# Optimization experiments

Measured on AMD Instinct MI355X. Metric: run time of the kernel, lower is better.

## Reference

```python
import jax, jax.numpy as jnp
import numpy as np
from jax import lax

NALGOS = 64
NTASKS = 1024
LX_LEN = 512
TASK_DIFFICULTY_SCALE = 1.0


def setup_inputs() -> dict:
    key = jax.random.key(0)
    k1, k2, k3, k4, k5, k6 = jax.random.split(key, 6)
    lx = jax.random.randint(k1, (LX_LEN,), 0, NTASKS)
    # task similarity in [-1, 1] as in the original (np.random.random * 2 - 1)
    task_matrix = jax.random.uniform(k2, (NTASKS, NTASKS), dtype=jnp.float32) * 2.0 - 1.0
    # difficulty in (0, 1); offset slightly away from 0 for numerical sanity of result/difficulty
    task_difficulty = jax.random.uniform(k3, (NTASKS,), dtype=jnp.float32, minval=0.05, maxval=1.0)
    alg_efficiency = 0.5 + 0.02 * jax.random.normal(k4, (NALGOS,), dtype=jnp.float32)
    alg_memory = 0.5 + 0.10 * jax.random.normal(k5, (NALGOS,), dtype=jnp.float32)
    alg_experience_boost = 0.5 + 0.02 * jax.random.normal(k6, (NALGOS,), dtype=jnp.float32)
    return {
        "lx": lx,
        "task_matrix": task_matrix,
        "task_difficulty": task_difficulty,
        "alg_efficiency": alg_efficiency,
        "alg_memory": alg_memory,
        "alg_experience_boost": alg_experience_boost,
    }


def _performance(lx, task_matrix, task_difficulty, alg_efficiency, alg_memory, alg_experience_boost):
    nalgos = alg_efficiency.shape[0]
    ntasks = task_matrix.shape[0]
    dtype = task_matrix.dtype
    diff = task_difficulty * TASK_DIFFICULTY_SCALE  # [T]

    eff = alg_efficiency[:, None]          # [A,1]
    mem = alg_memory[:, None]              # [A,1]
    boost = alg_experience_boost[:, None]  # [A,1]

    def step(carry, task):
        result, sig = carry                 # each [A,T]
        row = task_matrix[task]             # [T] similarity of current lx task to every task2
        prior_perf = sig[:, task][:, None]  # [A,1] sig of current lx task at previous step
        result_next = result * mem + row[None, :] * (eff + prior_perf * boost)
        sig_next = jax.nn.sigmoid(result_next / diff[None, :]) * 2.0 - 1.0
        return (result_next, sig_next), sig_next

    init = (jnp.zeros((nalgos, ntasks), dtype), jnp.zeros((nalgos, ntasks), dtype))
    _, sig_steps = lax.scan(step, init, lx)  # [L,A,T]
    sig_steps = jnp.transpose(sig_steps, (1, 2, 0))  # [A,T,L]
    # prepend the zero initial step -> [A,T,L+1], matching torch output layout
    zero0 = jnp.zeros((nalgos, ntasks, 1), dtype)
    return jnp.concatenate([zero0, sig_steps], axis=-1)


def reference(lx, task_matrix, task_difficulty, alg_efficiency, alg_memory, alg_experience_boost):
    return _performance(lx, task_matrix, task_difficulty, alg_efficiency, alg_memory, alg_experience_boost)
```

## Files before the change

### kernel.cpp

```cpp
#include <hip/hip_runtime.h>

#define NALGOS 64
#define NTASKS 1024
#define LXLEN  512
#define TOUT   (LXLEN + 1)
#define PROWS  (LXLEN + 8)

__device__ __forceinline__ float rdlane(float v, int lane) {
    return __int_as_float(__builtin_amdgcn_readlane(__float_as_int(v), lane));
}

__global__ __launch_bounds__(256) void phase0_kernel(
    const int* __restrict__ lx, const float* __restrict__ tm,
    float* __restrict__ P)
{
    const int t = blockIdx.x;
    const int i = threadIdx.x;
    if (t < LXLEN) {
        const int row = lx[t] * NTASKS;
        P[t * LXLEN + i]       = tm[row + lx[i]];
        P[t * LXLEN + i + 256] = tm[row + lx[i + 256]];
    } else {
        P[t * LXLEN + i]       = 0.f;
        P[t * LXLEN + i + 256] = 0.f;
    }
}

__global__ __launch_bounds__(64) void phase1_kernel(
    const int*   __restrict__ lx,
    const float* __restrict__ P,
    const float* __restrict__ diff,
    const float* __restrict__ eff_g,
    const float* __restrict__ mem_g,
    const float* __restrict__ boost_g,
    float*       __restrict__ coef_out)
{
    const int a = blockIdx.x, lane = threadIdx.x;

    float nk[8]; float V[8];
    #pragma unroll
    for (int k = 0; k < 8; ++k) {
        const int tsk = lx[lane + 64 * k];
        nk[k] = -1.4426950408889634f / diff[tsk];
        V[k] = 0.f;
    }
    const float eff = eff_g[a], mem = mem_g[a], boost = boost_g[a];

    float G[8][8];
    #pragma unroll
    for (int d = 0; d < 8; ++d)
        #pragma unroll
        for (int k = 0; k < 8; ++k)
            G[d][k] = P[d * LXLEN + 64 * k + lane];

    float coef = eff;
    float* cout = coef_out + (size_t)a * LXLEN;

    #pragma unroll
    for (int q = 0; q < 8; ++q) {
        float cbuf = 0.f;
        for (int g = 0; g < 8; ++g) {
            const int tb = q * 64 + g * 8;
            #pragma unroll
            for (int j = 0; j < 8; ++j) {
                const float p = V[q] * nk[q];
                float x = rdlane(p, g * 8 + j);
                x = fminf(fmaxf(x, -126.f), 126.f);
                const float e = __builtin_exp2f(x);
                const float u = (1.f - e) * __builtin_amdgcn_rcpf(1.f + e);
                coef = __builtin_fmaf(u, boost, eff);
                cbuf = (lane == g * 8 + j) ? coef : cbuf;
                #pragma unroll
                for (int k = q; k < 8; ++k)
                    V[k] = __builtin_fmaf(V[k], mem, G[j][k] * coef);
                const float* rp = P + (tb + j + 8) * LXLEN + lane;
                #pragma unroll
                for (int k = q; k < 8; ++k)
                    G[j][k] = rp[64 * k];
            }
        }
        cout[q * 64 + lane] = cbuf;
    }
}

__global__ __launch_bounds__(256, 4) void phase2_kernel(
    const int*   __restrict__ lx,
    const float* __restrict__ tm,
    const float* __restrict__ diff,
    const float* __restrict__ mem_g,
    const float* __restrict__ coef,
    float*       __restrict__ out)
{
    const int b = blockIdx.x;
    const int a = b >> 4, c = (b >> 2) & 3;
    const int n = ((b & 3) << 8) | threadIdx.x;
    const int t_begin = (c == 0) ? 0 : (c - 1) * 128;
    const int warm    = (c == 0) ? 0 : 128;
    const int len     = warm + 128;

    __shared__ __align__(16) int   task_sh[272 + 16];
    __shared__ __align__(16) float coef_sh[272 + 16];
    for (int i = threadIdx.x; i < len + 16; i += 256) {
        const int t = t_begin + i;
        task_sh[i] = (t < LXLEN) ? lx[t] : 0;
        coef_sh[i] = (t < LXLEN) ? coef[a * LXLEN + t] : 0.f;
    }

    const float mem   = mem_g[a];
    const float negkd = -1.4426950408889634f / diff[n];
    float* outp = out + ((size_t)a * NTASKS + n) * TOUT;
    float r = 0.f;
    __syncthreads();

    float rbuf[16];
    #pragma unroll
    for (int j = 0; j < 16; ++j) {
        const int tk = __builtin_amdgcn_readfirstlane(task_sh[j]);
        rbuf[j] = tm[(size_t)tk * NTASKS + n];
    }

    for (int base = 0; base < warm; base += 16) {
        float nbuf[16];
        #pragma unroll
        for (int j = 0; j < 16; ++j) {
            const int tk = __builtin_amdgcn_readfirstlane(task_sh[base + 16 + j]);
            nbuf[j] = tm[(size_t)tk * NTASKS + n];
        }
        #pragma unroll
        for (int v = 0; v < 4; ++v) {
            const float4 cq = *(const float4*)&coef_sh[base + 4 * v];
            r = __builtin_fmaf(r, mem, rbuf[4 * v + 0] * cq.x);
            r = __builtin_fmaf(r, mem, rbuf[4 * v + 1] * cq.y);
            r = __builtin_fmaf(r, mem, rbuf[4 * v + 2] * cq.z);
            r = __builtin_fmaf(r, mem, rbuf[4 * v + 3] * cq.w);
        }
        #pragma unroll
        for (int j = 0; j < 16; ++j) rbuf[j] = nbuf[j];
    }

    if (c == 0) outp[0] = 0.f;
    float* op = outp + t_begin + warm + 1;

    for (int base = warm; base < len; base += 16) {
        float nbuf[16];
        #pragma unroll
        for (int j = 0; j < 16; ++j) {
            const int tk = __builtin_amdgcn_readfirstlane(task_sh[base + 16 + j]);
            nbuf[j] = tm[(size_t)tk * NTASKS + n];
        }
        float sb[16];
        #pragma unroll
        for (int v = 0; v < 4; ++v) {
            const float4 cq = *(const float4*)&coef_sh[base + 4 * v];
            const float cf[4] = { cq.x, cq.y, cq.z, cq.w };
            #pragma unroll
            for (int u = 0; u < 4; ++u) {
                const int j = 4 * v + u;
                r = __builtin_fmaf(r, mem, rbuf[j] * cf[u]);
                float x = r * negkd;
                x = fminf(fmaxf(x, -126.f), 126.f);
                const float e = __builtin_exp2f(x);
                sb[j] = (1.f - e) * __builtin_amdgcn_rcpf(1.f + e);
            }
        }
        float* o = op + (base - warm);
        #pragma unroll
        for (int j = 0; j < 16; ++j) o[j] = sb[j];
        #pragma unroll
        for (int j = 0; j < 16; ++j) rbuf[j] = nbuf[j];
    }
}

__global__ __launch_bounds__(1024) void fused_fallback_kernel(
    const int* __restrict__ lx, const float* __restrict__ tm,
    const float* __restrict__ diff, const float* __restrict__ eff_g,
    const float* __restrict__ mem_g, const float* __restrict__ boost_g,
    float* __restrict__ out)
{
    const int a = blockIdx.x, n = threadIdx.x;
    __shared__ int lx_sh[LXLEN];
    __shared__ float sbuf[2];
    if (n < LXLEN) lx_sh[n] = lx[n];
    if (n == 0) sbuf[0] = 0.0f;
    const float eff = eff_g[a], mem = mem_g[a], boost = boost_g[a];
    const float negkd = -1.4426950408889634f / diff[n];
    float* outp = out + ((size_t)a * NTASKS + n) * TOUT;
    outp[0] = 0.0f;
    float r = 0.0f;
    __syncthreads();
    for (int t = 0; t < LXLEN; ++t) {
        const int task = lx_sh[t];
        const float s = sbuf[t & 1];
        const float coef = __builtin_fmaf(s, boost, eff);
        const float row = tm[task * NTASKS + n];
        r = __builtin_fmaf(r, mem, row * coef);
        float x = r * negkd;
        x = fminf(fmaxf(x, -126.0f), 126.0f);
        const float e = __builtin_exp2f(x);
        const float sig = (1.0f - e) * __builtin_amdgcn_rcpf(1.0f + e);
        outp[t + 1] = sig;
        if (t + 1 < LXLEN && n == lx_sh[t + 1]) sbuf[(t + 1) & 1] = sig;
        __syncthreads();
    }
}

extern "C" void kernel_launch(void* const* d_in, const int* in_sizes, int n_in,
                              void* d_out, int out_size, void* d_ws, size_t ws_size,
                              hipStream_t stream) {
    const int*   lx    = (const int*)  d_in[0];
    const float* tm    = (const float*)d_in[1];
    const float* diff  = (const float*)d_in[2];
    const float* eff   = (const float*)d_in[3];
    const float* mem   = (const float*)d_in[4];
    const float* boost = (const float*)d_in[5];
    float* out = (float*)d_out;

    const size_t coef_elems = (size_t)NALGOS * LXLEN;
    const size_t P_elems    = (size_t)PROWS * LXLEN;
    const size_t need_bytes = (coef_elems + P_elems) * sizeof(float);

    if (ws_size >= need_bytes) {
        float* coef = (float*)d_ws;
        float* P    = coef + coef_elems;
        phase0_kernel<<<dim3(PROWS), dim3(256), 0, stream>>>(lx, tm, P);
        phase1_kernel<<<dim3(NALGOS), dim3(64), 0, stream>>>(
            lx, P, diff, eff, mem, boost, coef);
        phase2_kernel<<<dim3(NALGOS * 16), dim3(256), 0, stream>>>(
            lx, tm, diff, mem, coef, out);
    } else {
        fused_fallback_kernel<<<dim3(NALGOS), dim3(NTASKS), 0, stream>>>(
            lx, tm, diff, eff, mem, boost, out);
    }
}
```

Measured before the change: 265.3 us.

## Deepen phase1 prefetch, split phase2 into more chunks, align output stores via LDS ring

Phase1 now prefetches 16 rows of P ahead instead of 8, which hides more global-load latency in the serial coefficient recurrence at the cost of more registers. Phase2 splits the time axis into 8 chunks of 64 steps instead of 4 of 128, doubling the grid for more parallelism and raising occupancy hints, though later chunks recompute up to 128 warm-up steps. Output rows of 513 floats are misaligned, so results now pass through a per-thread shared-memory ring buffer and are written as aligned float4 stores rather than scalar stores.

```diff
diff --git a/kernel.cpp b/kernel.cpp
--- a/kernel.cpp
+++ b/kernel.cpp
@@ -4,7 +4,8 @@
 #define NTASKS 1024
 #define LXLEN  512
 #define TOUT   (LXLEN + 1)
-#define PROWS  (LXLEN + 8)
+#define PDEPTH 16
+#define PROWS  (LXLEN + PDEPTH)
 
 __device__ __forceinline__ float rdlane(float v, int lane) {
     return __int_as_float(__builtin_amdgcn_readlane(__float_as_int(v), lane));
@@ -46,9 +47,9 @@
     }
     const float eff = eff_g[a], mem = mem_g[a], boost = boost_g[a];
 
-    float G[8][8];
-    #pragma unroll
-    for (int d = 0; d < 8; ++d)
+    float G[PDEPTH][8];
+    #pragma unroll
+    for (int d = 0; d < PDEPTH; ++d)
         #pragma unroll
         for (int k = 0; k < 8; ++k)
             G[d][k] = P[d * LXLEN + 64 * k + lane];
@@ -59,31 +60,36 @@
     #pragma unroll
     for (int q = 0; q < 8; ++q) {
         float cbuf = 0.f;
-        for (int g = 0; g < 8; ++g) {
-            const int tb = q * 64 + g * 8;
-            #pragma unroll
-            for (int j = 0; j < 8; ++j) {
-                const float p = V[q] * nk[q];
-                float x = rdlane(p, g * 8 + j);
-                x = fminf(fmaxf(x, -126.f), 126.f);
-                const float e = __builtin_exp2f(x);
-                const float u = (1.f - e) * __builtin_amdgcn_rcpf(1.f + e);
-                coef = __builtin_fmaf(u, boost, eff);
-                cbuf = (lane == g * 8 + j) ? coef : cbuf;
+        for (int gg = 0; gg < 4; ++gg) {
+            #pragma unroll
+            for (int h = 0; h < 2; ++h) {
+                const int g  = 2 * gg + h;
+                const int jb = h << 3;
+                const int tb = q * 64 + g * 8;
                 #pragma unroll
-                for (int k = q; k < 8; ++k)
-                    V[k] = __builtin_fmaf(V[k], mem, G[j][k] * coef);
-                const float* rp = P + (tb + j + 8) * LXLEN + lane;
-                #pragma unroll
-                for (int k = q; k < 8; ++k)
-                    G[j][k] = rp[64 * k];
+                for (int j = 0; j < 8; ++j) {
+                    const float p = V[q] * nk[q];
+                    float x = rdlane(p, g * 8 + j);
+                    x = fminf(fmaxf(x, -126.f), 126.f);
+                    const float e = __builtin_exp2f(x);
+                    const float u = (1.f - e) * __builtin_amdgcn_rcpf(1.f + e);
+                    coef = __builtin_fmaf(u, boost, eff);
+                    cbuf = (lane == g * 8 + j) ? coef : cbuf;
+                    #pragma unroll
+                    for (int k = q; k < 8; ++k)
+                        V[k] = __builtin_fmaf(V[k], mem, G[jb + j][k] * coef);
+                    const float* rp = P + (tb + j + PDEPTH) * LXLEN + lane;
+                    #pragma unroll
+                    for (int k = q; k < 8; ++k)
+                        G[jb + j][k] = rp[64 * k];
+                }
             }
         }
         cout[q * 64 + lane] = cbuf;
     }
 }
 
-__global__ __launch_bounds__(256, 4) void phase2_kernel(
+__global__ __launch_bounds__(256, 7) void phase2_kernel(
     const int*   __restrict__ lx,
     const float* __restrict__ tm,
     const float* __restrict__ diff,
@@ -92,16 +98,19 @@
     float*       __restrict__ out)
 {
     const int b = blockIdx.x;
-    const int a = b >> 4, c = (b >> 2) & 3;
+    const int a = b >> 5;
+    const int c = (b >> 2) & 7;
     const int n = ((b & 3) << 8) | threadIdx.x;
-    const int t_begin = (c == 0) ? 0 : (c - 1) * 128;
-    const int warm    = (c == 0) ? 0 : 128;
-    const int len     = warm + 128;
-
-    __shared__ __align__(16) int   task_sh[272 + 16];
-    __shared__ __align__(16) float coef_sh[272 + 16];
+    const int warm = (c >= 2) ? 128 : 64 * c;
+    const int t0   = 64 * c - warm;
+    const int len  = warm + 64;
+
+    __shared__ __align__(16) int   task_sh[216];
+    __shared__ __align__(16) float coef_sh[216];
+    __shared__ __align__(16) float ring[16 * 257];
+
     for (int i = threadIdx.x; i < len + 16; i += 256) {
-        const int t = t_begin + i;
+        const int t = t0 + i;
         task_sh[i] = (t < LXLEN) ? lx[t] : 0;
         coef_sh[i] = (t < LXLEN) ? coef[a * LXLEN + t] : 0.f;
     }
@@ -110,6 +119,11 @@
     const float negkd = -1.4426950408889634f / diff[n];
     float* outp = out + ((size_t)a * NTASKS + n) * TOUT;
     float r = 0.f;
+    float* ringc = ring + threadIdx.x;
+
+    const int phi = (n + 1) & 15;
+    const int hp  = 16 - phi;
+
     __syncthreads();
 
     float rbuf[16];
@@ -139,9 +153,11 @@
     }
 
     if (c == 0) outp[0] = 0.f;
-    float* op = outp + t_begin + warm + 1;
-
-    for (int base = warm; base < len; base += 16) {
+    float* op = outp + 64 * c + 1;
+
+    #pragma unroll
+    for (int kk = 0; kk < 4; ++kk) {
+        const int base = warm + 16 * kk;
         float nbuf[16];
         #pragma unroll
         for (int j = 0; j < 16; ++j) {
@@ -163,12 +179,39 @@
                 sb[j] = (1.f - e) * __builtin_amdgcn_rcpf(1.f + e);
             }
         }
-        float* o = op + (base - warm);
-        #pragma unroll
-        for (int j = 0; j < 16; ++j) o[j] = sb[j];
+
+        if (kk == 0) {
+            #pragma unroll
+            for (int j = 0; j < 16; ++j)
+                if (j < hp) op[j] = sb[j];
+            #pragma unroll
+            for (int j = 0; j < 16; ++j)
+                if (j >= hp) ringc[(j - hp) * 257] = sb[j];
+        } else {
+            #pragma unroll
+            for (int j = 0; j < 16; ++j)
+                if (j < hp) ringc[(j + phi) * 257] = sb[j];
+            float* dst = op + hp + 16 * (kk - 1);
+            #pragma unroll
+            for (int qd = 0; qd < 4; ++qd) {
+                float4 w;
+                w.x = ringc[(4 * qd + 0) * 257];
+                w.y = ringc[(4 * qd + 1) * 257];
+                w.z = ringc[(4 * qd + 2) * 257];
+                w.w = ringc[(4 * qd + 3) * 257];
+                ((float4*)dst)[qd] = w;
+            }
+            #pragma unroll
+            for (int j = 0; j < 16; ++j)
+                if (j >= hp) ringc[(j - hp) * 257] = sb[j];
+        }
         #pragma unroll
         for (int j = 0; j < 16; ++j) rbuf[j] = nbuf[j];
     }
+
+    #pragma unroll
+    for (int j = 0; j < 16; ++j)
+        if (j < phi) op[hp + 48 + j] = ringc[j * 257];
 }
 
 __global__ __launch_bounds__(1024) void fused_fallback_kernel(
@@ -225,7 +268,7 @@
         phase0_kernel<<<dim3(PROWS), dim3(256), 0, stream>>>(lx, tm, P);
         phase1_kernel<<<dim3(NALGOS), dim3(64), 0, stream>>>(
             lx, P, diff, eff, mem, boost, coef);
-        phase2_kernel<<<dim3(NALGOS * 16), dim3(256), 0, stream>>>(
+        phase2_kernel<<<dim3(NALGOS * 32), dim3(256), 0, stream>>>(
             lx, tm, diff, mem, coef, out);
     } else {
         fused_fallback_kernel<<<dim3(NALGOS), dim3(NTASKS), 0, stream>>>(
```

Result: slower. 603.3 us (+127.4%).

## Stage phase2 outputs through LDS ring for coalesced stores and double time chunks

Applied to the files above, without the earlier changes.

Phase2 now splits the time axis into eight chunks of 64 steps instead of four of 128, doubling the grid, with shorter warmups for the early chunks. Each thread writes its sigmoid results into a shared-memory ring buffer, skewed per task index to line up with 64-byte boundaries. The block then transposes them so consecutive lanes store consecutive time steps of one output row, replacing the strided per-thread row writes. The cost is extra LDS traffic, more complex index and edge handling, and more redundant warmup recurrence work across the added chunks.

```diff
diff --git a/kernel.cpp b/kernel.cpp
--- a/kernel.cpp
+++ b/kernel.cpp
@@ -91,25 +91,39 @@
     const float* __restrict__ coef,
     float*       __restrict__ out)
 {
-    const int b = blockIdx.x;
-    const int a = b >> 4, c = (b >> 2) & 3;
-    const int n = ((b & 3) << 8) | threadIdx.x;
-    const int t_begin = (c == 0) ? 0 : (c - 1) * 128;
-    const int warm    = (c == 0) ? 0 : 128;
-    const int len     = warm + 128;
-
-    __shared__ __align__(16) int   task_sh[272 + 16];
-    __shared__ __align__(16) float coef_sh[272 + 16];
-    for (int i = threadIdx.x; i < len + 16; i += 256) {
-        const int t = t_begin + i;
-        task_sh[i] = (t < LXLEN) ? lx[t] : 0;
-        coef_sh[i] = (t < LXLEN) ? coef[a * LXLEN + t] : 0.f;
+    const int b   = blockIdx.x;
+    const int a   = b >> 5;
+    const int c   = (b >> 2) & 7;
+    const int seg = b & 3;
+    const int tid = threadIdx.x;
+    const int n   = (seg << 8) | tid;
+
+    const int warm = (c >= 2) ? 128 : 64 * c;
+    const int t0   = 64 * c - 1 - warm;
+
+    __shared__ __align__(16) int   task_sh[224];
+    __shared__ __align__(16) float coef_sh[224];
+    __shared__ __align__(16) float ring[32 * 257];
+
+    const int nfill = warm + 96;
+    for (int i = tid; i < nfill; i += 256) {
+        const int t = t0 + i;
+        const bool ok = (t >= 0) && (t < LXLEN);
+        task_sh[i] = ok ? lx[t] : 0;
+        coef_sh[i] = ok ? coef[a * LXLEN + t] : 0.f;
     }
 
     const float mem   = mem_g[a];
     const float negkd = -1.4426950408889634f / diff[n];
-    float* outp = out + ((size_t)a * NTASKS + n) * TOUT;
-    float r = 0.f;
+    const int   d     = (16 - (n & 15)) & 15;
+    float* rowp = out + ((size_t)a * NTASKS + n) * TOUT;
+    float  r    = 0.f;
+    float* ringc = ring + tid;
+
+    const int wb = tid & 192;
+    const int lq = tid & 15;
+    const int qq = (tid >> 4) & 3;
+
     __syncthreads();
 
     float rbuf[16];
@@ -138,36 +152,56 @@
         for (int j = 0; j < 16; ++j) rbuf[j] = nbuf[j];
     }
 
-    if (c == 0) outp[0] = 0.f;
-    float* op = outp + t_begin + warm + 1;
-
-    for (int base = warm; base < len; base += 16) {
+    #pragma unroll
+    for (int rr = 0; rr < 5; ++rr) {
+        const int base = warm + 16 * rr;
         float nbuf[16];
         #pragma unroll
         for (int j = 0; j < 16; ++j) {
             const int tk = __builtin_amdgcn_readfirstlane(task_sh[base + 16 + j]);
             nbuf[j] = tm[(size_t)tk * NTASKS + n];
         }
-        float sb[16];
         #pragma unroll
         for (int v = 0; v < 4; ++v) {
             const float4 cq = *(const float4*)&coef_sh[base + 4 * v];
             const float cf[4] = { cq.x, cq.y, cq.z, cq.w };
             #pragma unroll
-            for (int u = 0; u < 4; ++u) {
-                const int j = 4 * v + u;
-                r = __builtin_fmaf(r, mem, rbuf[j] * cf[u]);
+            for (int u4 = 0; u4 < 4; ++u4) {
+                const int j = 4 * v + u4;
+                r = __builtin_fmaf(r, mem, rbuf[j] * cf[u4]);
                 float x = r * negkd;
                 x = fminf(fmaxf(x, -126.f), 126.f);
                 const float e = __builtin_exp2f(x);
-                sb[j] = (1.f - e) * __builtin_amdgcn_rcpf(1.f + e);
+                const float sig = (1.f - e) * __builtin_amdgcn_rcpf(1.f + e);
+                ringc[((16 * rr + j - d) & 31) * 257] = sig;
+                if (c == 0 && rr == 0 && j < d) rowp[j] = sig;
             }
         }
-        float* o = op + (base - warm);
-        #pragma unroll
-        for (int j = 0; j < 16; ++j) o[j] = sb[j];
+        if (rr >= 1) {
+            const int g    = rr - 1;
+            const int sb16 = (g & 1) << 4;
+            #pragma unroll
+            for (int sub = 0; sub < 16; ++sub) {
+                const int tau = wb + 4 * sub + qq;
+                const int nn  = (seg << 8) | tau;
+                const int dd  = (16 - qq - 4 * (sub & 3)) & 15;
+                const float vv = ring[(sb16 + lq) * 257 + tau];
+                if (!(c == 7 && g == 3 && dd > 1)) {
+                    out[((size_t)a * NTASKS + nn) * TOUT
+                        + 64 * c + dd + 16 * g + lq] = vv;
+                }
+            }
+        }
         #pragma unroll
         for (int j = 0; j < 16; ++j) rbuf[j] = nbuf[j];
+    }
+
+    if (c == 7) {
+        const int tt0 = (d == 1) ? 513 : ((d == 0) ? 512 : 496 + d);
+        #pragma unroll
+        for (int u = 496; u <= 512; ++u) {
+            if (u >= tt0) rowp[u] = ringc[(((u - 448) - d) & 31) * 257];
+        }
     }
 }
 
@@ -225,7 +259,7 @@
         phase0_kernel<<<dim3(PROWS), dim3(256), 0, stream>>>(lx, tm, P);
         phase1_kernel<<<dim3(NALGOS), dim3(64), 0, stream>>>(
             lx, P, diff, eff, mem, boost, coef);
-        phase2_kernel<<<dim3(NALGOS * 16), dim3(256), 0, stream>>>(
+        phase2_kernel<<<dim3(NALGOS * 32), dim3(256), 0, stream>>>(
             lx, tm, diff, mem, coef, out);
     } else {
         fused_fallback_kernel<<<dim3(NALGOS), dim3(NTASKS), 0, stream>>>(
```

After: 225.9 us. -14.9%, faster.
